# Performance work log

Measured on AMD Instinct MI355X. Metric: run time of the kernel, lower is better.

The kernel has to match this reference:

```python
import jax, jax.numpy as jnp
import numpy as np

N, E, F, H, G, C = 50000, 600000, 128, 128, 64, 2


def setup_inputs() -> dict:
    key = jax.random.key(0)
    ks = jax.random.split(key, 12)
    s = lambda d: np.float32(1.0 / np.sqrt(d))
    return {
        "x": jax.random.normal(ks[0], (N, F), jnp.float32),
        "edge_index": jax.random.randint(ks[1], (2, E), 0, N),
        "batch": jnp.sort(jax.random.randint(ks[2], (N,), 0, G)),
        "W1": jax.random.normal(ks[3], (F, H), jnp.float32) * s(F),
        "b1": jnp.zeros((H,), jnp.float32),
        "W2": jax.random.normal(ks[4], (H, H), jnp.float32) * s(H),
        "b2": jnp.zeros((H,), jnp.float32),
        "Wl1": jax.random.normal(ks[5], (H, 128), jnp.float32) * s(H),
        "bl1": jnp.zeros((128,), jnp.float32),
        "Wl2": jax.random.normal(ks[6], (128, 128), jnp.float32) * s(128),
        "bl2": jnp.zeros((128,), jnp.float32),
        "Wo": jax.random.normal(ks[7], (128, C), jnp.float32) * s(128),
        "bo": jnp.zeros((C,), jnp.float32),
    }


def _gcn_conv(x, src, dst, norm, W, b, n_nodes):
    # PyG GCNConv: transform then normalized scatter-add aggregation
    h = x @ W                                  # [N, H]
    msg = h[src] * norm[:, None]               # gather + scale, [E+N, H]
    out = jax.ops.segment_sum(msg, dst, num_segments=n_nodes)
    return out + b


def reference(x, edge_index, batch, W1, b1, W2, b2, Wl1, bl1, Wl2, bl2, Wo, bo):
    n = x.shape[0]
    loop = jnp.arange(n)
    src = jnp.concatenate([edge_index[0], loop])  # add self-loops
    dst = jnp.concatenate([edge_index[1], loop])
    deg = jax.ops.segment_sum(jnp.ones_like(src, dtype=x.dtype), dst, num_segments=n)
    dinv = jnp.where(deg > 0, jax.lax.rsqrt(deg), 0.0)
    norm = dinv[src] * dinv[dst]               # D^-1/2 (A+I) D^-1/2

    h = jax.nn.relu(_gcn_conv(x, src, dst, norm, W1, b1, n))
    h = _gcn_conv(h, src, dst, norm, W2, b2, n)
    g = jax.ops.segment_max(h, batch, num_segments=G)  # global max pool -> [G, H]
    g = jax.nn.relu(g @ Wl1 + bl1)
    g = jax.nn.relu(g @ Wl2 + bl2)
    # dropout p=0.5 is identity in eval mode
    return jax.nn.softmax(g @ Wo + bo, axis=1)
```

## Files before the change

### kernel.cpp

```cpp
#include <hip/hip_runtime.h>
#include <hip/hip_bf16.h>
#include <cfloat>
#include <cmath>

#define HF 128
#define DEGCAP 48

typedef __attribute__((ext_vector_type(8))) short bf16x8;
typedef __attribute__((ext_vector_type(4))) float f32x4;

__device__ __forceinline__ unsigned short f2bf(float x) {
    union { float f; unsigned u; } v; v.f = x;
    unsigned r = v.u + 0x7FFFu + ((v.u >> 16) & 1u);
    return (unsigned short)(r >> 16);
}
__device__ __forceinline__ float bf2f(unsigned short b) {
    union { unsigned u; float f; } v; v.u = ((unsigned)b) << 16;
    return v.f;
}

__device__ __forceinline__ unsigned enc_f(float x) {
    unsigned u = __float_as_uint(x);
    return (u & 0x80000000u) ? ~u : (u | 0x80000000u);
}
__device__ __forceinline__ float dec_f(unsigned e) {
    unsigned u = (e & 0x80000000u) ? (e & 0x7FFFFFFFu) : ~e;
    return __uint_as_float(u);
}

__global__ void k_init(int* __restrict__ cnt, unsigned* __restrict__ genc,
                       int N, int GF) {
    int i = blockIdx.x * blockDim.x + threadIdx.x;
    if (i < N) cnt[i] = 0;
    if (i < GF) genc[i] = 0x007FFFFFu;
}

__global__ void k_fill(const int* __restrict__ src, const int* __restrict__ dst,
                       int* __restrict__ cnt, unsigned short* __restrict__ csr, int E) {
    int i = blockIdx.x * blockDim.x + threadIdx.x;
    if (i < E) {
        int d = dst[i];
        int c = atomicAdd(&cnt[d], 1);
        if (c < DEGCAP) csr[d * DEGCAP + c] = (unsigned short)src[i];
    }
}

__global__ __launch_bounds__(256) void k_gemm_mfma(
        const void* __restrict__ Ain, int a_is_bf16,
        const float* __restrict__ W, const int* __restrict__ cnt,
        unsigned short* __restrict__ Y, int M) {
    __shared__ unsigned short Wt[128 * 136];
    int tid = threadIdx.x;
    {
        int n4 = (tid & 31) * 4;
        int kr = tid >> 5;
        for (int k = kr; k < HF; k += 8) {
            float4 w = *(const float4*)&W[(size_t)k * HF + n4];
            Wt[(n4 + 0) * 136 + k] = f2bf(w.x);
            Wt[(n4 + 1) * 136 + k] = f2bf(w.y);
            Wt[(n4 + 2) * 136 + k] = f2bf(w.z);
            Wt[(n4 + 3) * 136 + k] = f2bf(w.w);
        }
    }
    __syncthreads();

    int wave = tid >> 6, lane = tid & 63;
    int l15 = lane & 15, quad = lane >> 4;
    int rbase = blockIdx.x * 128 + wave * 32;

    f32x4 acc[2][8];
    #pragma unroll
    for (int mt = 0; mt < 2; ++mt)
        #pragma unroll
        for (int nt = 0; nt < 8; ++nt)
            acc[mt][nt] = (f32x4){0.f, 0.f, 0.f, 0.f};

    #pragma unroll
    for (int kc = 0; kc < 4; ++kc) {
        int kk = kc * 32 + quad * 8;
        bf16x8 a[2];
        #pragma unroll
        for (int mt = 0; mt < 2; ++mt) {
            int r = rbase + mt * 16 + l15;
            bf16x8 t = {};
            if (r < M) {
                if (a_is_bf16) {
                    const unsigned short* A = (const unsigned short*)Ain;
                    t = *(const bf16x8*)&A[(size_t)r * HF + kk];
                } else {
                    const float* A = (const float*)Ain;
                    float4 f0 = *(const float4*)&A[(size_t)r * HF + kk];
                    float4 f1 = *(const float4*)&A[(size_t)r * HF + kk + 4];
                    t[0] = (short)f2bf(f0.x); t[1] = (short)f2bf(f0.y);
                    t[2] = (short)f2bf(f0.z); t[3] = (short)f2bf(f0.w);
                    t[4] = (short)f2bf(f1.x); t[5] = (short)f2bf(f1.y);
                    t[6] = (short)f2bf(f1.z); t[7] = (short)f2bf(f1.w);
                }
            }
            a[mt] = t;
        }
        #pragma unroll
        for (int nt = 0; nt < 8; ++nt) {
            int n = nt * 16 + l15;
            bf16x8 b = *(const bf16x8*)&Wt[n * 136 + kk];
            #pragma unroll
            for (int mt = 0; mt < 2; ++mt)
                acc[mt][nt] = __builtin_amdgcn_mfma_f32_16x16x32_bf16(
                    a[mt], b, acc[mt][nt], 0, 0, 0);
        }
    }
    #pragma unroll
    for (int mt = 0; mt < 2; ++mt) {
        #pragma unroll
        for (int reg = 0; reg < 4; ++reg) {
            int r = rbase + mt * 16 + quad * 4 + reg;
            if (r < M) {
                float di = rsqrtf((float)(cnt[r] + 1));
                #pragma unroll
                for (int nt = 0; nt < 8; ++nt)
                    Y[(size_t)r * HF + nt * 16 + l15] = f2bf(acc[mt][nt][reg] * di);
            }
        }
    }
}

__device__ __forceinline__ void acc_row(float* acc, uint4 p) {
    acc[0] += bf2f((unsigned short)(p.x & 0xFFFFu));
    acc[1] += bf2f((unsigned short)(p.x >> 16));
    acc[2] += bf2f((unsigned short)(p.y & 0xFFFFu));
    acc[3] += bf2f((unsigned short)(p.y >> 16));
    acc[4] += bf2f((unsigned short)(p.z & 0xFFFFu));
    acc[5] += bf2f((unsigned short)(p.z >> 16));
    acc[6] += bf2f((unsigned short)(p.w & 0xFFFFu));
    acc[7] += bf2f((unsigned short)(p.w >> 16));
}
__device__ __forceinline__ uint4 row_ld(const unsigned short* __restrict__ hxs,
                                        int row, int lane) {
    return *(const uint4*)&hxs[(size_t)row * HF + lane * 8];
}

__device__ __forceinline__ void agg_core(const unsigned short* __restrict__ hxs,
                                         const unsigned short* __restrict__ row,
                                         int deg, int node, int lane, float* acc) {
    #pragma unroll
    for (int j = 0; j < 8; ++j) acc[j] = 0.f;
    uint4 self = row_ld(hxs, node, lane);
    int e = 0;
    for (; e + 8 <= deg; e += 8) {
        uint4 p[8];
        #pragma unroll
        for (int u = 0; u < 8; ++u) p[u] = row_ld(hxs, (int)row[e + u], lane);
        #pragma unroll
        for (int u = 0; u < 8; ++u) acc_row(acc, p[u]);
    }
    if (e + 4 <= deg) {
        uint4 p[4];
        #pragma unroll
        for (int u = 0; u < 4; ++u) p[u] = row_ld(hxs, (int)row[e + u], lane);
        #pragma unroll
        for (int u = 0; u < 4; ++u) acc_row(acc, p[u]);
        e += 4;
    }
    for (; e < deg; ++e) acc_row(acc, row_ld(hxs, (int)row[e], lane));
    acc_row(acc, self);
}

__global__ __launch_bounds__(256) void k_agg1(
        const unsigned short* __restrict__ hxs, const unsigned short* __restrict__ csr,
        const int* __restrict__ cnt, const float* __restrict__ bias,
        unsigned short* __restrict__ out, int N) {
    int tid  = threadIdx.x;
    int node = blockIdx.x * 16 + (tid >> 4);
    int lane = tid & 15;
    if (node >= N) return;
    int c = cnt[node];
    int deg = min(c, DEGCAP);
    float di = rsqrtf((float)(c + 1));
    float acc[8];
    agg_core(hxs, &csr[(size_t)node * DEGCAP], deg, node, lane, acc);
    const float* b = &bias[lane * 8];
    ushort4 o0, o1;
    o0.x = f2bf(fmaxf(acc[0] * di + b[0], 0.f));
    o0.y = f2bf(fmaxf(acc[1] * di + b[1], 0.f));
    o0.z = f2bf(fmaxf(acc[2] * di + b[2], 0.f));
    o0.w = f2bf(fmaxf(acc[3] * di + b[3], 0.f));
    o1.x = f2bf(fmaxf(acc[4] * di + b[4], 0.f));
    o1.y = f2bf(fmaxf(acc[5] * di + b[5], 0.f));
    o1.z = f2bf(fmaxf(acc[6] * di + b[6], 0.f));
    o1.w = f2bf(fmaxf(acc[7] * di + b[7], 0.f));
    *(ushort4*)&out[(size_t)node * HF + lane * 8 + 0] = o0;
    *(ushort4*)&out[(size_t)node * HF + lane * 8 + 4] = o1;
}

__global__ __launch_bounds__(256) void k_agg2(
        const unsigned short* __restrict__ hxs, const unsigned short* __restrict__ csr,
        const int* __restrict__ cnt, const float* __restrict__ bias,
        unsigned short* __restrict__ out, int N) {
    int tid  = threadIdx.x;
    int node = blockIdx.x * 16 + (tid >> 4);
    int lane = tid & 15;
    if (node >= N) return;
    int c = cnt[node];
    int deg = min(c, DEGCAP);
    float di = rsqrtf((float)(c + 1));
    float acc[8];
    agg_core(hxs, &csr[(size_t)node * DEGCAP], deg, node, lane, acc);
    const float* b = &bias[lane * 8];
    ushort4 o0, o1;
    o0.x = f2bf(acc[0] * di + b[0]);
    o0.y = f2bf(acc[1] * di + b[1]);
    o0.z = f2bf(acc[2] * di + b[2]);
    o0.w = f2bf(acc[3] * di + b[3]);
    o1.x = f2bf(acc[4] * di + b[4]);
    o1.y = f2bf(acc[5] * di + b[5]);
    o1.z = f2bf(acc[6] * di + b[6]);
    o1.w = f2bf(acc[7] * di + b[7]);
    *(ushort4*)&out[(size_t)node * HF + lane * 8 + 0] = o0;
    *(ushort4*)&out[(size_t)node * HF + lane * 8 + 4] = o1;
}

__global__ __launch_bounds__(128) void k_pool(
        const unsigned short* __restrict__ h, const int* __restrict__ batch,
        unsigned* __restrict__ genc, int N) {
    int f  = threadIdx.x;
    int r0 = blockIdx.x * 32;
    int rend = min(r0 + 32, N);
    int cur = batch[r0];
    float m = -FLT_MAX;
    for (int r = r0; r < rend; ++r) {
        int b   = batch[r];
        float v = bf2f(h[(size_t)r * HF + f]);
        if (b != cur) {
            atomicMax(&genc[cur * HF + f], enc_f(m));
            m = -FLT_MAX; cur = b;
        }
        m = fmaxf(m, v);
    }
    atomicMax(&genc[cur * HF + f], enc_f(m));
}

__global__ __launch_bounds__(128) void k_mlp(
        const unsigned* __restrict__ genc,
        const float* __restrict__ Wl1, const float* __restrict__ bl1,
        const float* __restrict__ Wl2, const float* __restrict__ bl2,
        const float* __restrict__ Wo,  const float* __restrict__ bo,
        float* __restrict__ out) {
    __shared__ float s0[HF], s1[HF], r0[HF], r1[HF];
    int f = threadIdx.x, row = blockIdx.x;
    s0[f] = dec_f(genc[row * HF + f]);
    __syncthreads();
    float a = bl1[f];
    #pragma unroll 8
    for (int k = 0; k < HF; ++k) a += s0[k] * Wl1[k * HF + f];
    a = fmaxf(a, 0.f);
    s1[f] = a;
    __syncthreads();
    float a2 = bl2[f];
    #pragma unroll 8
    for (int k = 0; k < HF; ++k) a2 += s1[k] * Wl2[k * HF + f];
    a2 = fmaxf(a2, 0.f);
    r0[f] = a2 * Wo[f * 2 + 0];
    r1[f] = a2 * Wo[f * 2 + 1];
    __syncthreads();
    for (int s = 64; s > 0; s >>= 1) {
        if (f < s) { r0[f] += r0[f + s]; r1[f] += r1[f + s]; }
        __syncthreads();
    }
    if (f == 0) {
        float l0 = r0[0] + bo[0], l1 = r1[0] + bo[1];
        float mx = fmaxf(l0, l1);
        float e0 = expf(l0 - mx), e1 = expf(l1 - mx);
        float inv = 1.f / (e0 + e1);
        out[row * 2 + 0] = e0 * inv;
        out[row * 2 + 1] = e1 * inv;
    }
}

extern "C" void kernel_launch(void* const* d_in, const int* in_sizes, int n_in,
                              void* d_out, int out_size, void* d_ws, size_t ws_size,
                              hipStream_t stream) {
    const float* x    = (const float*)d_in[0];
    const int*   edge = (const int*)  d_in[1];
    const int*   batch= (const int*)  d_in[2];
    const float* W1   = (const float*)d_in[3];
    const float* b1   = (const float*)d_in[4];
    const float* W2   = (const float*)d_in[5];
    const float* b2   = (const float*)d_in[6];
    const float* Wl1  = (const float*)d_in[7];
    const float* bl1  = (const float*)d_in[8];
    const float* Wl2  = (const float*)d_in[9];
    const float* bl2  = (const float*)d_in[10];
    const float* Wo   = (const float*)d_in[11];
    const float* bo   = (const float*)d_in[12];
    float* out = (float*)d_out;

    int N = in_sizes[2];
    int E = in_sizes[1] / 2;
    int G = out_size / 2;
    int GF = G * HF;

    char* ws = (char*)d_ws;
    auto alloc = [&](size_t bytes) -> void* {
        void* p = ws;
        ws += (bytes + 255) & ~(size_t)255;
        return p;
    };
    unsigned short* bufX = (unsigned short*)alloc((size_t)N * HF * 2);
    unsigned short* bufH = (unsigned short*)alloc((size_t)N * HF * 2);
    int*            cnt  = (int*)           alloc((size_t)N * 4);
    unsigned short* csr  = (unsigned short*)alloc((size_t)N * DEGCAP * 2);
    unsigned*       genc = (unsigned*)      alloc((size_t)GF * 4);

    const int* srcv = edge;
    const int* dstv = edge + E;

    int initN = (N > GF ? N : GF);
    k_init<<<(initN + 255) / 256, 256, 0, stream>>>(cnt, genc, N, GF);
    k_fill<<<(E + 255) / 256,     256, 0, stream>>>(srcv, dstv, cnt, csr, E);

    k_gemm_mfma<<<(N + 127) / 128, 256, 0, stream>>>(x,    0, W1, cnt, bufX, N);
    k_agg1     <<<(N + 15)  / 16,  256, 0, stream>>>(bufX, csr, cnt, b1, bufH, N);
    k_gemm_mfma<<<(N + 127) / 128, 256, 0, stream>>>(bufH, 1, W2, cnt, bufX, N);
    k_agg2     <<<(N + 15)  / 16,  256, 0, stream>>>(bufX, csr, cnt, b2, bufH, N);

    k_pool<<<(N + 31) / 32, 128, 0, stream>>>(bufH, batch, genc, N);
    k_mlp <<<G,             128, 0, stream>>>(genc, Wl1, bl1, Wl2, bl2, Wo, bo, out);
}
```

Measured before the change: 234.3 us.

## Fuse layer-1 aggregation with layer-2 GEMM and fuse pooling into MLP

Layer-1 neighbor aggregation is merged with the second transform. Each wave gathers 16 nodes' rows into registers, applies bias, ReLU and normalization, then feeds them straight into MFMA against W2 staged in LDS. This removes one full N×128 bf16 write/read and one launch. Global max pooling now runs per graph inside the MLP kernel, binary-searching the sorted batch array, which drops the atomic encode/decode pass and the genc init. The trade-off is that the fused gather uses one lane per node with 32 accumulators (more registers, less coalescing per lane), and pooling is serialized across only G blocks.

```diff
diff --git a/kernel.cpp b/kernel.cpp
--- a/kernel.cpp
+++ b/kernel.cpp
@@ -19,20 +19,9 @@
     return v.f;
 }
 
-__device__ __forceinline__ unsigned enc_f(float x) {
-    unsigned u = __float_as_uint(x);
-    return (u & 0x80000000u) ? ~u : (u | 0x80000000u);
-}
-__device__ __forceinline__ float dec_f(unsigned e) {
-    unsigned u = (e & 0x80000000u) ? (e & 0x7FFFFFFFu) : ~e;
-    return __uint_as_float(u);
-}
-
-__global__ void k_init(int* __restrict__ cnt, unsigned* __restrict__ genc,
-                       int N, int GF) {
+__global__ void k_init(int* __restrict__ cnt, int N) {
     int i = blockIdx.x * blockDim.x + threadIdx.x;
     if (i < N) cnt[i] = 0;
-    if (i < GF) genc[i] = 0x007FFFFFu;
 }
 
 __global__ void k_fill(const int* __restrict__ src, const int* __restrict__ dst,
@@ -45,23 +34,25 @@
     }
 }
 
+__device__ __forceinline__ void stage_wt(const float* __restrict__ W,
+                                         unsigned short* __restrict__ Wt, int tid) {
+    int n4 = (tid & 31) * 4;
+    int kr = tid >> 5;
+    for (int k = kr; k < HF; k += 8) {
+        float4 w = *(const float4*)&W[(size_t)k * HF + n4];
+        Wt[(n4 + 0) * 136 + k] = f2bf(w.x);
+        Wt[(n4 + 1) * 136 + k] = f2bf(w.y);
+        Wt[(n4 + 2) * 136 + k] = f2bf(w.z);
+        Wt[(n4 + 3) * 136 + k] = f2bf(w.w);
+    }
+}
+
 __global__ __launch_bounds__(256) void k_gemm_mfma(
-        const void* __restrict__ Ain, int a_is_bf16,
-        const float* __restrict__ W, const int* __restrict__ cnt,
-        unsigned short* __restrict__ Y, int M) {
+        const float* __restrict__ X, const float* __restrict__ W,
+        const int* __restrict__ cnt, unsigned short* __restrict__ Y, int M) {
     __shared__ unsigned short Wt[128 * 136];
     int tid = threadIdx.x;
-    {
-        int n4 = (tid & 31) * 4;
-        int kr = tid >> 5;
-        for (int k = kr; k < HF; k += 8) {
-            float4 w = *(const float4*)&W[(size_t)k * HF + n4];
-            Wt[(n4 + 0) * 136 + k] = f2bf(w.x);
-            Wt[(n4 + 1) * 136 + k] = f2bf(w.y);
-            Wt[(n4 + 2) * 136 + k] = f2bf(w.z);
-            Wt[(n4 + 3) * 136 + k] = f2bf(w.w);
-        }
-    }
+    stage_wt(W, Wt, tid);
     __syncthreads();
 
     int wave = tid >> 6, lane = tid & 63;
@@ -82,27 +73,20 @@
         #pragma unroll
         for (int mt = 0; mt < 2; ++mt) {
             int r = rbase + mt * 16 + l15;
-            bf16x8 t = {};
+            bf16x8 v = {};
             if (r < M) {
-                if (a_is_bf16) {
-                    const unsigned short* A = (const unsigned short*)Ain;
-                    t = *(const bf16x8*)&A[(size_t)r * HF + kk];
-                } else {
-                    const float* A = (const float*)Ain;
-                    float4 f0 = *(const float4*)&A[(size_t)r * HF + kk];
-                    float4 f1 = *(const float4*)&A[(size_t)r * HF + kk + 4];
-                    t[0] = (short)f2bf(f0.x); t[1] = (short)f2bf(f0.y);
-                    t[2] = (short)f2bf(f0.z); t[3] = (short)f2bf(f0.w);
-                    t[4] = (short)f2bf(f1.x); t[5] = (short)f2bf(f1.y);
-                    t[6] = (short)f2bf(f1.z); t[7] = (short)f2bf(f1.w);
-                }
+                float4 f0 = *(const float4*)&X[(size_t)r * HF + kk];
+                float4 f1 = *(const float4*)&X[(size_t)r * HF + kk + 4];
+                v[0] = (short)f2bf(f0.x); v[1] = (short)f2bf(f0.y);
+                v[2] = (short)f2bf(f0.z); v[3] = (short)f2bf(f0.w);
+                v[4] = (short)f2bf(f1.x); v[5] = (short)f2bf(f1.y);
+                v[6] = (short)f2bf(f1.z); v[7] = (short)f2bf(f1.w);
             }
-            a[mt] = t;
+            a[mt] = v;
         }
         #pragma unroll
         for (int nt = 0; nt < 8; ++nt) {
-            int n = nt * 16 + l15;
-            bf16x8 b = *(const bf16x8*)&Wt[n * 136 + kk];
+            bf16x8 b = *(const bf16x8*)&Wt[(nt * 16 + l15) * 136 + kk];
             #pragma unroll
             for (int mt = 0; mt < 2; ++mt)
                 acc[mt][nt] = __builtin_amdgcn_mfma_f32_16x16x32_bf16(
@@ -134,64 +118,100 @@
     acc[6] += bf2f((unsigned short)(p.w & 0xFFFFu));
     acc[7] += bf2f((unsigned short)(p.w >> 16));
 }
+
+__global__ __launch_bounds__(256) void k_agg1_gemm2(
+        const unsigned short* __restrict__ bufX, const unsigned short* __restrict__ csr,
+        const int* __restrict__ cnt, const float* __restrict__ b1,
+        const float* __restrict__ W2, unsigned short* __restrict__ out, int N) {
+    __shared__ unsigned short Wt[128 * 136];
+    int tid = threadIdx.x;
+    stage_wt(W2, Wt, tid);
+    __syncthreads();
+
+    int wave = tid >> 6, lane = tid & 63;
+    int l15 = lane & 15, quad = lane >> 4;
+    int nbase = blockIdx.x * 64 + wave * 16;
+    int node  = nbase + l15;
+
+    float acc[32];
+    #pragma unroll
+    for (int j = 0; j < 32; ++j) acc[j] = 0.f;
+
+    int c = 0, deg = 0;
+    if (node < N) { c = cnt[node]; deg = min(c, DEGCAP); }
+
+    int q8 = quad * 8;
+    auto gat = [&](int r) {
+        const unsigned short* base = &bufX[(size_t)r * HF + q8];
+        uint4 p0 = *(const uint4*)(base + 0);
+        uint4 p1 = *(const uint4*)(base + 32);
+        uint4 p2 = *(const uint4*)(base + 64);
+        uint4 p3 = *(const uint4*)(base + 96);
+        acc_row(&acc[0],  p0);
+        acc_row(&acc[8],  p1);
+        acc_row(&acc[16], p2);
+        acc_row(&acc[24], p3);
+    };
+
+    if (node < N) {
+        gat(node);
+        const unsigned short* row = &csr[(size_t)node * DEGCAP];
+        int e = 0;
+        for (; e + 2 <= deg; e += 2) {
+            const unsigned short* a0 = &bufX[(size_t)row[e]     * HF + q8];
+            const unsigned short* a1 = &bufX[(size_t)row[e + 1] * HF + q8];
+            uint4 p0 = *(const uint4*)(a0 + 0),  p1 = *(const uint4*)(a0 + 32);
+            uint4 p2 = *(const uint4*)(a0 + 64), p3 = *(const uint4*)(a0 + 96);
+            uint4 p4 = *(const uint4*)(a1 + 0),  p5 = *(const uint4*)(a1 + 32);
+            uint4 p6 = *(const uint4*)(a1 + 64), p7 = *(const uint4*)(a1 + 96);
+            acc_row(&acc[0], p0);  acc_row(&acc[8], p1);
+            acc_row(&acc[16], p2); acc_row(&acc[24], p3);
+            acc_row(&acc[0], p4);  acc_row(&acc[8], p5);
+            acc_row(&acc[16], p6); acc_row(&acc[24], p7);
+        }
+        if (e < deg) gat(row[e]);
+    }
+
+    float di = (node < N) ? rsqrtf((float)(c + 1)) : 0.f;
+    bf16x8 afrag[4];
+    #pragma unroll
+    for (int kc = 0; kc < 4; ++kc) {
+        #pragma unroll
+        for (int j = 0; j < 8; ++j) {
+            float h = fmaxf(acc[kc * 8 + j] * di + b1[kc * 32 + q8 + j], 0.f);
+            afrag[kc][j] = (short)f2bf(h);
+        }
+    }
+
+    f32x4 cacc[8];
+    #pragma unroll
+    for (int nt = 0; nt < 8; ++nt) cacc[nt] = (f32x4){0.f, 0.f, 0.f, 0.f};
+    #pragma unroll
+    for (int kc = 0; kc < 4; ++kc) {
+        int kk = kc * 32 + q8;
+        #pragma unroll
+        for (int nt = 0; nt < 8; ++nt) {
+            bf16x8 b = *(const bf16x8*)&Wt[(nt * 16 + l15) * 136 + kk];
+            cacc[nt] = __builtin_amdgcn_mfma_f32_16x16x32_bf16(
+                afrag[kc], b, cacc[nt], 0, 0, 0);
+        }
+    }
+    #pragma unroll
+    for (int reg = 0; reg < 4; ++reg) {
+        int r = nbase + quad * 4 + reg;
+        if (r < N) {
+            float d2 = rsqrtf((float)(cnt[r] + 1));
+            #pragma unroll
+            for (int nt = 0; nt < 8; ++nt)
+                out[(size_t)r * HF + nt * 16 + l15] = f2bf(cacc[nt][reg] * d2);
+        }
+    }
+}
+
 __device__ __forceinline__ uint4 row_ld(const unsigned short* __restrict__ hxs,
                                         int row, int lane) {
     return *(const uint4*)&hxs[(size_t)row * HF + lane * 8];
 }
-
-__device__ __forceinline__ void agg_core(const unsigned short* __restrict__ hxs,
-                                         const unsigned short* __restrict__ row,
-                                         int deg, int node, int lane, float* acc) {
-    #pragma unroll
-    for (int j = 0; j < 8; ++j) acc[j] = 0.f;
-    uint4 self = row_ld(hxs, node, lane);
-    int e = 0;
-    for (; e + 8 <= deg; e += 8) {
-        uint4 p[8];
-        #pragma unroll
-        for (int u = 0; u < 8; ++u) p[u] = row_ld(hxs, (int)row[e + u], lane);
-        #pragma unroll
-        for (int u = 0; u < 8; ++u) acc_row(acc, p[u]);
-    }
-    if (e + 4 <= deg) {
-        uint4 p[4];
-        #pragma unroll
-        for (int u = 0; u < 4; ++u) p[u] = row_ld(hxs, (int)row[e + u], lane);
-        #pragma unroll
-        for (int u = 0; u < 4; ++u) acc_row(acc, p[u]);
-        e += 4;
-    }
-    for (; e < deg; ++e) acc_row(acc, row_ld(hxs, (int)row[e], lane));
-    acc_row(acc, self);
-}
-
-__global__ __launch_bounds__(256) void k_agg1(
-        const unsigned short* __restrict__ hxs, const unsigned short* __restrict__ csr,
-        const int* __restrict__ cnt, const float* __restrict__ bias,
-        unsigned short* __restrict__ out, int N) {
-    int tid  = threadIdx.x;
-    int node = blockIdx.x * 16 + (tid >> 4);
-    int lane = tid & 15;
-    if (node >= N) return;
-    int c = cnt[node];
-    int deg = min(c, DEGCAP);
-    float di = rsqrtf((float)(c + 1));
-    float acc[8];
-    agg_core(hxs, &csr[(size_t)node * DEGCAP], deg, node, lane, acc);
-    const float* b = &bias[lane * 8];
-    ushort4 o0, o1;
-    o0.x = f2bf(fmaxf(acc[0] * di + b[0], 0.f));
-    o0.y = f2bf(fmaxf(acc[1] * di + b[1], 0.f));
-    o0.z = f2bf(fmaxf(acc[2] * di + b[2], 0.f));
-    o0.w = f2bf(fmaxf(acc[3] * di + b[3], 0.f));
-    o1.x = f2bf(fmaxf(acc[4] * di + b[4], 0.f));
-    o1.y = f2bf(fmaxf(acc[5] * di + b[5], 0.f));
-    o1.z = f2bf(fmaxf(acc[6] * di + b[6], 0.f));
-    o1.w = f2bf(fmaxf(acc[7] * di + b[7], 0.f));
-    *(ushort4*)&out[(size_t)node * HF + lane * 8 + 0] = o0;
-    *(ushort4*)&out[(size_t)node * HF + lane * 8 + 4] = o1;
-}
-
 __global__ __launch_bounds__(256) void k_agg2(
         const unsigned short* __restrict__ hxs, const unsigned short* __restrict__ csr,
         const int* __restrict__ cnt, const float* __restrict__ bias,
@@ -204,7 +224,27 @@
     int deg = min(c, DEGCAP);
     float di = rsqrtf((float)(c + 1));
     float acc[8];
-    agg_core(hxs, &csr[(size_t)node * DEGCAP], deg, node, lane, acc);
+    #pragma unroll
+    for (int j = 0; j < 8; ++j) acc[j] = 0.f;
+    acc_row(acc, row_ld(hxs, node, lane));
+    const unsigned short* row = &csr[(size_t)node * DEGCAP];
+    int e = 0;
+    for (; e + 8 <= deg; e += 8) {
+        uint4 p[8];
+        #pragma unroll
+        for (int u = 0; u < 8; ++u) p[u] = row_ld(hxs, (int)row[e + u], lane);
+        #pragma unroll
+        for (int u = 0; u < 8; ++u) acc_row(acc, p[u]);
+    }
+    if (e + 4 <= deg) {
+        uint4 p[4];
+        #pragma unroll
+        for (int u = 0; u < 4; ++u) p[u] = row_ld(hxs, (int)row[e + u], lane);
+        #pragma unroll
+        for (int u = 0; u < 4; ++u) acc_row(acc, p[u]);
+        e += 4;
+    }
+    for (; e < deg; ++e) acc_row(acc, row_ld(hxs, (int)row[e], lane));
     const float* b = &bias[lane * 8];
     ushort4 o0, o1;
     o0.x = f2bf(acc[0] * di + b[0]);
@@ -219,35 +259,30 @@
     *(ushort4*)&out[(size_t)node * HF + lane * 8 + 4] = o1;
 }
 
-__global__ __launch_bounds__(128) void k_pool(
-        const unsigned short* __restrict__ h, const int* __restrict__ batch,
-        unsigned* __restrict__ genc, int N) {
-    int f  = threadIdx.x;
-    int r0 = blockIdx.x * 32;
-    int rend = min(r0 + 32, N);
-    int cur = batch[r0];
-    float m = -FLT_MAX;
-    for (int r = r0; r < rend; ++r) {
-        int b   = batch[r];
-        float v = bf2f(h[(size_t)r * HF + f]);
-        if (b != cur) {
-            atomicMax(&genc[cur * HF + f], enc_f(m));
-            m = -FLT_MAX; cur = b;
-        }
-        m = fmaxf(m, v);
-    }
-    atomicMax(&genc[cur * HF + f], enc_f(m));
-}
-
-__global__ __launch_bounds__(128) void k_mlp(
-        const unsigned* __restrict__ genc,
+__global__ __launch_bounds__(128) void k_poolmlp(
+        const unsigned short* __restrict__ h, const int* __restrict__ batch, int N,
         const float* __restrict__ Wl1, const float* __restrict__ bl1,
         const float* __restrict__ Wl2, const float* __restrict__ bl2,
         const float* __restrict__ Wo,  const float* __restrict__ bo,
         float* __restrict__ out) {
+    int f = threadIdx.x, g = blockIdx.x;
+    int lo, hi;
+    { int a = 0, b = N; while (a < b) { int m = (a + b) >> 1; if (batch[m] < g) a = m + 1; else b = m; } lo = a; }
+    { int a = lo, b = N; while (a < b) { int m = (a + b) >> 1; if (batch[m] < g + 1) a = m + 1; else b = m; } hi = a; }
+
+    float m0 = -FLT_MAX, m1 = -FLT_MAX, m2 = -FLT_MAX, m3 = -FLT_MAX;
+    int r = lo;
+    for (; r + 4 <= hi; r += 4) {
+        m0 = fmaxf(m0, bf2f(h[(size_t)(r + 0) * HF + f]));
+        m1 = fmaxf(m1, bf2f(h[(size_t)(r + 1) * HF + f]));
+        m2 = fmaxf(m2, bf2f(h[(size_t)(r + 2) * HF + f]));
+        m3 = fmaxf(m3, bf2f(h[(size_t)(r + 3) * HF + f]));
+    }
+    for (; r < hi; ++r) m0 = fmaxf(m0, bf2f(h[(size_t)r * HF + f]));
+    float m = fmaxf(fmaxf(m0, m1), fmaxf(m2, m3));
+
     __shared__ float s0[HF], s1[HF], r0[HF], r1[HF];
-    int f = threadIdx.x, row = blockIdx.x;
-    s0[f] = dec_f(genc[row * HF + f]);
+    s0[f] = m;
     __syncthreads();
     float a = bl1[f];
     #pragma unroll 8
@@ -271,8 +306,8 @@
         float mx = fmaxf(l0, l1);
         float e0 = expf(l0 - mx), e1 = expf(l1 - mx);
         float inv = 1.f / (e0 + e1);
-        out[row * 2 + 0] = e0 * inv;
-        out[row * 2 + 1] = e1 * inv;
+        out[g * 2 + 0] = e0 * inv;
+        out[g * 2 + 1] = e1 * inv;
     }
 }
 
@@ -297,7 +332,6 @@
     int N = in_sizes[2];
     int E = in_sizes[1] / 2;
     int G = out_size / 2;
-    int GF = G * HF;
 
     char* ws = (char*)d_ws;
     auto alloc = [&](size_t bytes) -> void* {
@@ -306,23 +340,19 @@
         return p;
     };
     unsigned short* bufX = (unsigned short*)alloc((size_t)N * HF * 2);
-    unsigned short* bufH = (unsigned short*)alloc((size_t)N * HF * 2);
+    unsigned short* bufY = (unsigned short*)alloc((size_t)N * HF * 2);
     int*            cnt  = (int*)           alloc((size_t)N * 4);
     unsigned short* csr  = (unsigned short*)alloc((size_t)N * DEGCAP * 2);
-    unsigned*       genc = (unsigned*)      alloc((size_t)GF * 4);
 
     const int* srcv = edge;
     const int* dstv = edge + E;
 
-    int initN = (N > GF ? N : GF);
-    k_init<<<(initN + 255) / 256, 256, 0, stream>>>(cnt, genc, N, GF);
-    k_fill<<<(E + 255) / 256,     256, 0, stream>>>(srcv, dstv, cnt, csr, E);
-
-    k_gemm_mfma<<<(N + 127) / 128, 256, 0, stream>>>(x,    0, W1, cnt, bufX, N);
-    k_agg1     <<<(N + 15)  / 16,  256, 0, stream>>>(bufX, csr, cnt, b1, bufH, N);
-    k_gemm_mfma<<<(N + 127) / 128, 256, 0, stream>>>(bufH, 1, W2, cnt, bufX, N);
-    k_agg2     <<<(N + 15)  / 16,  256, 0, stream>>>(bufX, csr, cnt, b2, bufH, N);
-
-    k_pool<<<(N + 31) / 32, 128, 0, stream>>>(bufH, batch, genc, N);
-    k_mlp <<<G,             128, 0, stream>>>(genc, Wl1, bl1, Wl2, bl2, Wo, bo, out);
-}
+    k_init<<<(N + 255) / 256, 256, 0, stream>>>(cnt, N);
+    k_fill<<<(E + 255) / 256, 256, 0, stream>>>(srcv, dstv, cnt, csr, E);
+
+    k_gemm_mfma <<<(N + 127) / 128, 256, 0, stream>>>(x, W1, cnt, bufX, N);
+    k_agg1_gemm2<<<(N + 63)  / 64,  256, 0, stream>>>(bufX, csr, cnt, b1, W2, bufY, N);
+    k_agg2      <<<(N + 15)  / 16,  256, 0, stream>>>(bufY, csr, cnt, b2, bufX, N);
+
+    k_poolmlp<<<G, 128, 0, stream>>>(bufX, batch, N, Wl1, bl1, Wl2, bl2, Wo, bo, out);
+}
```

Measured after the change: 293.6 us. 25.3% more time.

## Fuse CSR fill with first GEMM and move source normalization into aggregation

Applied to the files above, without the earlier changes.

The first GEMM no longer needs the final degree counts, so the scatter-fill of the CSR and the first MFMA GEMM now run as disjoint block ranges of a single launch. The source-side D^-1/2 scaling for layer 1 moves into the first aggregation, which computes rsqrt of each neighbor's count on the fly. The separate init kernel becomes a single memset over a combined cnt/pool buffer, with the pool max sentinel changing from a fixed pattern to zero. This removes a launch and a serialization point and lets the atomic-heavy fill overlap the GEMM. In exchange, layer-1 aggregation does an extra per-edge gather of cnt and an rsqrt.

```diff
diff --git a/kernel.cpp b/kernel.cpp
--- a/kernel.cpp
+++ b/kernel.cpp
@@ -5,6 +5,7 @@
 
 #define HF 128
 #define DEGCAP 48
+#define EPB 4096
 
 typedef __attribute__((ext_vector_type(8))) short bf16x8;
 typedef __attribute__((ext_vector_type(4))) float f32x4;
@@ -28,40 +29,99 @@
     return __uint_as_float(u);
 }
 
-__global__ void k_init(int* __restrict__ cnt, unsigned* __restrict__ genc,
-                       int N, int GF) {
-    int i = blockIdx.x * blockDim.x + threadIdx.x;
-    if (i < N) cnt[i] = 0;
-    if (i < GF) genc[i] = 0x007FFFFFu;
-}
-
-__global__ void k_fill(const int* __restrict__ src, const int* __restrict__ dst,
-                       int* __restrict__ cnt, unsigned short* __restrict__ csr, int E) {
-    int i = blockIdx.x * blockDim.x + threadIdx.x;
-    if (i < E) {
-        int d = dst[i];
-        int c = atomicAdd(&cnt[d], 1);
-        if (c < DEGCAP) csr[d * DEGCAP + c] = (unsigned short)src[i];
-    }
-}
-
-__global__ __launch_bounds__(256) void k_gemm_mfma(
-        const void* __restrict__ Ain, int a_is_bf16,
-        const float* __restrict__ W, const int* __restrict__ cnt,
+__device__ __forceinline__ void stage_wt(const float* __restrict__ W,
+                                         unsigned short* __restrict__ Wt, int tid) {
+    int n4 = (tid & 31) * 4;
+    int kr = tid >> 5;
+    for (int k = kr; k < HF; k += 8) {
+        float4 w = *(const float4*)&W[(size_t)k * HF + n4];
+        Wt[(n4 + 0) * 136 + k] = f2bf(w.x);
+        Wt[(n4 + 1) * 136 + k] = f2bf(w.y);
+        Wt[(n4 + 2) * 136 + k] = f2bf(w.z);
+        Wt[(n4 + 3) * 136 + k] = f2bf(w.w);
+    }
+}
+
+__global__ __launch_bounds__(256) void k_fill_gemm1(
+        const int* __restrict__ src, const int* __restrict__ dst,
+        int* __restrict__ cnt, unsigned short* __restrict__ csr, int E, int FB,
+        const float* __restrict__ X, const float* __restrict__ W,
         unsigned short* __restrict__ Y, int M) {
     __shared__ unsigned short Wt[128 * 136];
     int tid = threadIdx.x;
-    {
-        int n4 = (tid & 31) * 4;
-        int kr = tid >> 5;
-        for (int k = kr; k < HF; k += 8) {
-            float4 w = *(const float4*)&W[(size_t)k * HF + n4];
-            Wt[(n4 + 0) * 136 + k] = f2bf(w.x);
-            Wt[(n4 + 1) * 136 + k] = f2bf(w.y);
-            Wt[(n4 + 2) * 136 + k] = f2bf(w.z);
-            Wt[(n4 + 3) * 136 + k] = f2bf(w.w);
-        }
-    }
+
+    if (blockIdx.x < FB) {
+        int e0 = blockIdx.x * EPB + tid;
+        int e1 = min(blockIdx.x * EPB + EPB, E);
+        for (int i = e0; i < e1; i += 256) {
+            int d = dst[i];
+            int c = atomicAdd(&cnt[d], 1);
+            if (c < DEGCAP) csr[d * DEGCAP + c] = (unsigned short)src[i];
+        }
+        return;
+    }
+
+    stage_wt(W, Wt, tid);
+    __syncthreads();
+
+    int wave = tid >> 6, lane = tid & 63;
+    int l15 = lane & 15, quad = lane >> 4;
+    int rbase = (blockIdx.x - FB) * 128 + wave * 32;
+
+    f32x4 acc[2][8];
+    #pragma unroll
+    for (int mt = 0; mt < 2; ++mt)
+        #pragma unroll
+        for (int nt = 0; nt < 8; ++nt)
+            acc[mt][nt] = (f32x4){0.f, 0.f, 0.f, 0.f};
+
+    #pragma unroll
+    for (int kc = 0; kc < 4; ++kc) {
+        int kk = kc * 32 + quad * 8;
+        bf16x8 a[2];
+        #pragma unroll
+        for (int mt = 0; mt < 2; ++mt) {
+            int r = rbase + mt * 16 + l15;
+            bf16x8 v = {};
+            if (r < M) {
+                float4 f0 = *(const float4*)&X[(size_t)r * HF + kk];
+                float4 f1 = *(const float4*)&X[(size_t)r * HF + kk + 4];
+                v[0] = (short)f2bf(f0.x); v[1] = (short)f2bf(f0.y);
+                v[2] = (short)f2bf(f0.z); v[3] = (short)f2bf(f0.w);
+                v[4] = (short)f2bf(f1.x); v[5] = (short)f2bf(f1.y);
+                v[6] = (short)f2bf(f1.z); v[7] = (short)f2bf(f1.w);
+            }
+            a[mt] = v;
+        }
+        #pragma unroll
+        for (int nt = 0; nt < 8; ++nt) {
+            bf16x8 b = *(const bf16x8*)&Wt[(nt * 16 + l15) * 136 + kk];
+            #pragma unroll
+            for (int mt = 0; mt < 2; ++mt)
+                acc[mt][nt] = __builtin_amdgcn_mfma_f32_16x16x32_bf16(
+                    a[mt], b, acc[mt][nt], 0, 0, 0);
+        }
+    }
+    #pragma unroll
+    for (int mt = 0; mt < 2; ++mt) {
+        #pragma unroll
+        for (int reg = 0; reg < 4; ++reg) {
+            int r = rbase + mt * 16 + quad * 4 + reg;
+            if (r < M) {
+                #pragma unroll
+                for (int nt = 0; nt < 8; ++nt)
+                    Y[(size_t)r * HF + nt * 16 + l15] = f2bf(acc[mt][nt][reg]);
+            }
+        }
+    }
+}
+
+__global__ __launch_bounds__(256) void k_gemm2(
+        const unsigned short* __restrict__ A, const float* __restrict__ W,
+        const int* __restrict__ cnt, unsigned short* __restrict__ Y, int M) {
+    __shared__ unsigned short Wt[128 * 136];
+    int tid = threadIdx.x;
+    stage_wt(W, Wt, tid);
     __syncthreads();
 
     int wave = tid >> 6, lane = tid & 63;
@@ -82,27 +142,13 @@
         #pragma unroll
         for (int mt = 0; mt < 2; ++mt) {
             int r = rbase + mt * 16 + l15;
-            bf16x8 t = {};
-            if (r < M) {
-                if (a_is_bf16) {
-                    const unsigned short* A = (const unsigned short*)Ain;
-                    t = *(const bf16x8*)&A[(size_t)r * HF + kk];
-                } else {
-                    const float* A = (const float*)Ain;
-                    float4 f0 = *(const float4*)&A[(size_t)r * HF + kk];
-                    float4 f1 = *(const float4*)&A[(size_t)r * HF + kk + 4];
-                    t[0] = (short)f2bf(f0.x); t[1] = (short)f2bf(f0.y);
-                    t[2] = (short)f2bf(f0.z); t[3] = (short)f2bf(f0.w);
-                    t[4] = (short)f2bf(f1.x); t[5] = (short)f2bf(f1.y);
-                    t[6] = (short)f2bf(f1.z); t[7] = (short)f2bf(f1.w);
-                }
-            }
-            a[mt] = t;
+            bf16x8 v = {};
+            if (r < M) v = *(const bf16x8*)&A[(size_t)r * HF + kk];
+            a[mt] = v;
         }
         #pragma unroll
         for (int nt = 0; nt < 8; ++nt) {
-            int n = nt * 16 + l15;
-            bf16x8 b = *(const bf16x8*)&Wt[n * 136 + kk];
+            bf16x8 b = *(const bf16x8*)&Wt[(nt * 16 + l15) * 136 + kk];
             #pragma unroll
             for (int mt = 0; mt < 2; ++mt)
                 acc[mt][nt] = __builtin_amdgcn_mfma_f32_16x16x32_bf16(
@@ -124,6 +170,10 @@
     }
 }
 
+__device__ __forceinline__ uint4 row_ld(const unsigned short* __restrict__ hxs,
+                                        int row, int lane) {
+    return *(const uint4*)&hxs[(size_t)row * HF + lane * 8];
+}
 __device__ __forceinline__ void acc_row(float* acc, uint4 p) {
     acc[0] += bf2f((unsigned short)(p.x & 0xFFFFu));
     acc[1] += bf2f((unsigned short)(p.x >> 16));
@@ -134,39 +184,19 @@
     acc[6] += bf2f((unsigned short)(p.w & 0xFFFFu));
     acc[7] += bf2f((unsigned short)(p.w >> 16));
 }
-__device__ __forceinline__ uint4 row_ld(const unsigned short* __restrict__ hxs,
-                                        int row, int lane) {
-    return *(const uint4*)&hxs[(size_t)row * HF + lane * 8];
-}
-
-__device__ __forceinline__ void agg_core(const unsigned short* __restrict__ hxs,
-                                         const unsigned short* __restrict__ row,
-                                         int deg, int node, int lane, float* acc) {
-    #pragma unroll
-    for (int j = 0; j < 8; ++j) acc[j] = 0.f;
-    uint4 self = row_ld(hxs, node, lane);
-    int e = 0;
-    for (; e + 8 <= deg; e += 8) {
-        uint4 p[8];
-        #pragma unroll
-        for (int u = 0; u < 8; ++u) p[u] = row_ld(hxs, (int)row[e + u], lane);
-        #pragma unroll
-        for (int u = 0; u < 8; ++u) acc_row(acc, p[u]);
-    }
-    if (e + 4 <= deg) {
-        uint4 p[4];
-        #pragma unroll
-        for (int u = 0; u < 4; ++u) p[u] = row_ld(hxs, (int)row[e + u], lane);
-        #pragma unroll
-        for (int u = 0; u < 4; ++u) acc_row(acc, p[u]);
-        e += 4;
-    }
-    for (; e < deg; ++e) acc_row(acc, row_ld(hxs, (int)row[e], lane));
-    acc_row(acc, self);
+__device__ __forceinline__ void acc_row_w(float* acc, uint4 p, float w) {
+    acc[0] += bf2f((unsigned short)(p.x & 0xFFFFu)) * w;
+    acc[1] += bf2f((unsigned short)(p.x >> 16)) * w;
+    acc[2] += bf2f((unsigned short)(p.y & 0xFFFFu)) * w;
+    acc[3] += bf2f((unsigned short)(p.y >> 16)) * w;
+    acc[4] += bf2f((unsigned short)(p.z & 0xFFFFu)) * w;
+    acc[5] += bf2f((unsigned short)(p.z >> 16)) * w;
+    acc[6] += bf2f((unsigned short)(p.w & 0xFFFFu)) * w;
+    acc[7] += bf2f((unsigned short)(p.w >> 16)) * w;
 }
 
 __global__ __launch_bounds__(256) void k_agg1(
-        const unsigned short* __restrict__ hxs, const unsigned short* __restrict__ csr,
+        const unsigned short* __restrict__ Z1, const unsigned short* __restrict__ csr,
         const int* __restrict__ cnt, const float* __restrict__ bias,
         unsigned short* __restrict__ out, int N) {
     int tid  = threadIdx.x;
@@ -177,7 +207,38 @@
     int deg = min(c, DEGCAP);
     float di = rsqrtf((float)(c + 1));
     float acc[8];
-    agg_core(hxs, &csr[(size_t)node * DEGCAP], deg, node, lane, acc);
+    #pragma unroll
+    for (int j = 0; j < 8; ++j) acc[j] = 0.f;
+    acc_row_w(acc, row_ld(Z1, node, lane), di);
+    const unsigned short* row = &csr[(size_t)node * DEGCAP];
+    int e = 0;
+    for (; e + 8 <= deg; e += 8) {
+        uint4 p[8]; float w[8];
+        #pragma unroll
+        for (int u = 0; u < 8; ++u) {
+            int s = (int)row[e + u];
+            p[u] = row_ld(Z1, s, lane);
+            w[u] = rsqrtf((float)(cnt[s] + 1));
+        }
+        #pragma unroll
+        for (int u = 0; u < 8; ++u) acc_row_w(acc, p[u], w[u]);
+    }
+    if (e + 4 <= deg) {
+        uint4 p[4]; float w[4];
+        #pragma unroll
+        for (int u = 0; u < 4; ++u) {
+            int s = (int)row[e + u];
+            p[u] = row_ld(Z1, s, lane);
+            w[u] = rsqrtf((float)(cnt[s] + 1));
+        }
+        #pragma unroll
+        for (int u = 0; u < 4; ++u) acc_row_w(acc, p[u], w[u]);
+        e += 4;
+    }
+    for (; e < deg; ++e) {
+        int s = (int)row[e];
+        acc_row_w(acc, row_ld(Z1, s, lane), rsqrtf((float)(cnt[s] + 1)));
+    }
     const float* b = &bias[lane * 8];
     ushort4 o0, o1;
     o0.x = f2bf(fmaxf(acc[0] * di + b[0], 0.f));
@@ -204,7 +265,27 @@
     int deg = min(c, DEGCAP);
     float di = rsqrtf((float)(c + 1));
     float acc[8];
-    agg_core(hxs, &csr[(size_t)node * DEGCAP], deg, node, lane, acc);
+    #pragma unroll
+    for (int j = 0; j < 8; ++j) acc[j] = 0.f;
+    acc_row(acc, row_ld(hxs, node, lane));
+    const unsigned short* row = &csr[(size_t)node * DEGCAP];
+    int e = 0;
+    for (; e + 8 <= deg; e += 8) {
+        uint4 p[8];
+        #pragma unroll
+        for (int u = 0; u < 8; ++u) p[u] = row_ld(hxs, (int)row[e + u], lane);
+        #pragma unroll
+        for (int u = 0; u < 8; ++u) acc_row(acc, p[u]);
+    }
+    if (e + 4 <= deg) {
+        uint4 p[4];
+        #pragma unroll
+        for (int u = 0; u < 4; ++u) p[u] = row_ld(hxs, (int)row[e + u], lane);
+        #pragma unroll
+        for (int u = 0; u < 4; ++u) acc_row(acc, p[u]);
+        e += 4;
+    }
+    for (; e < deg; ++e) acc_row(acc, row_ld(hxs, (int)row[e], lane));
     const float* b = &bias[lane * 8];
     ushort4 o0, o1;
     o0.x = f2bf(acc[0] * di + b[0]);
@@ -307,21 +388,25 @@
     };
     unsigned short* bufX = (unsigned short*)alloc((size_t)N * HF * 2);
     unsigned short* bufH = (unsigned short*)alloc((size_t)N * HF * 2);
-    int*            cnt  = (int*)           alloc((size_t)N * 4);
     unsigned short* csr  = (unsigned short*)alloc((size_t)N * DEGCAP * 2);
-    unsigned*       genc = (unsigned*)      alloc((size_t)GF * 4);
+    size_t cnt_span = ((size_t)N * 4 + 255) & ~(size_t)255;
+    char*  zbase    = (char*)alloc(cnt_span + (size_t)GF * 4);
+    int*      cnt   = (int*)zbase;
+    unsigned* genc  = (unsigned*)(zbase + cnt_span);
+    size_t    zlen  = cnt_span + (size_t)GF * 4;
 
     const int* srcv = edge;
     const int* dstv = edge + E;
 
-    int initN = (N > GF ? N : GF);
-    k_init<<<(initN + 255) / 256, 256, 0, stream>>>(cnt, genc, N, GF);
-    k_fill<<<(E + 255) / 256,     256, 0, stream>>>(srcv, dstv, cnt, csr, E);
-
-    k_gemm_mfma<<<(N + 127) / 128, 256, 0, stream>>>(x,    0, W1, cnt, bufX, N);
-    k_agg1     <<<(N + 15)  / 16,  256, 0, stream>>>(bufX, csr, cnt, b1, bufH, N);
-    k_gemm_mfma<<<(N + 127) / 128, 256, 0, stream>>>(bufH, 1, W2, cnt, bufX, N);
-    k_agg2     <<<(N + 15)  / 16,  256, 0, stream>>>(bufX, csr, cnt, b2, bufH, N);
+    hipMemsetAsync(zbase, 0, zlen, stream);
+
+    int FB = (E + EPB - 1) / EPB;
+    int GB = (N + 127) / 128;
+    k_fill_gemm1<<<FB + GB, 256, 0, stream>>>(srcv, dstv, cnt, csr, E, FB,
+                                              x, W1, bufX, N);
+    k_agg1 <<<(N + 15)  / 16,  256, 0, stream>>>(bufX, csr, cnt, b1, bufH, N);
+    k_gemm2<<<(N + 127) / 128, 256, 0, stream>>>(bufH, W2, cnt, bufX, N);
+    k_agg2 <<<(N + 15)  / 16,  256, 0, stream>>>(bufX, csr, cnt, b2, bufH, N);
 
     k_pool<<<(N + 31) / 32, 128, 0, stream>>>(bufH, batch, genc, N);
     k_mlp <<<G,             128, 0, stream>>>(genc, Wl1, bl1, Wl2, bl2, Wo, bo, out);
```

Result: faster. 221.5 us (-5.5%).
